# Kernel optimization log

Hardware: AMD Instinct MI355X
Metric: run time of the kernel (lower is better)

Reference implementation:

```python
import jax, jax.numpy as jnp
import numpy as np

T, H, I, E, Z, TOPK = 1024, 1024, 512, 32, 8, 4
ROUTED_SCALING = 1.0


def setup_inputs() -> dict:
    key = jax.random.key(0)
    k1, k2, k3, k4 = jax.random.split(key, 4)
    return {
        "hidden_states": jax.random.normal(k1, (T, H), jnp.float32),
        "router_w": jax.random.normal(k2, (E + Z, H), jnp.float32) * 0.02,
        "correction_bias": jnp.zeros((E + Z,), jnp.float32),
        "w_gate_up": jax.random.normal(k3, (E, 2 * I, H), jnp.float32) * 0.02,
        "w_down": jax.random.normal(k4, (E, H, I), jnp.float32) * 0.02,
        "top_k": TOPK,
    }


def reference(hidden_states, router_w, correction_bias, w_gate_up, w_down, top_k):
    # hidden_states: [T, H]; router_w: [E+Z, H]; w_gate_up: [E, 2I, H]; w_down: [E, H, I]
    t, h = hidden_states.shape
    e = w_gate_up.shape[0]
    i = w_down.shape[2]
    # --- router (float32, no bias; correction bias only affects selection) ---
    logits = jnp.einsum("th,eh->te", hidden_states.astype(jnp.float32), router_w)
    scores = jax.nn.softmax(logits, axis=-1)                     # [T, E+Z]
    _, idx = jax.lax.top_k(scores + correction_bias[None, :], top_k)  # [T, k]
    w = jnp.take_along_axis(scores, idx, axis=1) * ROUTED_SCALING     # renormalize=False
    # combine matrix [T, E+Z] (sparse top-k scattered dense)
    comb = jnp.zeros((t, scores.shape[1]), jnp.float32)
    comb = comb.at[jnp.arange(t)[:, None], idx].add(w)
    comb_routed = comb[:, :e].astype(hidden_states.dtype)        # [T, E]
    zero_w = comb[:, e:].sum(-1).astype(hidden_states.dtype)     # [T] identity zero-experts
    # --- grouped SiLU-gated expert MLPs (dense all-experts reference) ---
    gu = jnp.einsum("th,eih->eti", hidden_states, w_gate_up)     # [E, T, 2I]
    hmid = jax.nn.silu(gu[..., :i]) * gu[..., i:]                # [E, T, I]
    ye = jnp.einsum("eti,ehi->eth", hmid, w_down)                # [E, T, H]
    out = jnp.einsum("te,eth->th", comb_routed, ye)
    out = out + zero_w[:, None] * hidden_states
    return out
```

## Files before the change

### kernel.cpp

```cpp
#include <hip/hip_runtime.h>
#include <hip/hip_bf16.h>
#include <math.h>

#define TT   1024
#define HH   1024
#define II   512
#define EE   32
#define NE   40
#define TOPK 4
#define CAP  1024

#define GM  128
#define GNP 16
#define GK  32
#define KP  40
#define DN  32

typedef __attribute__((ext_vector_type(4))) short short4v;
typedef __attribute__((ext_vector_type(8))) short short8v;
typedef __attribute__((ext_vector_type(4))) float floatx4;

static __device__ __forceinline__ short f2bf(float f) {
    unsigned u = __float_as_uint(f);
    unsigned r = (u + 0x7fffu + ((u >> 16) & 1u)) >> 16;
    return (short)(r & 0xffffu);
}
static __device__ __forceinline__ float bf2f(short s) {
    return __uint_as_float(((unsigned)(unsigned short)s) << 16);
}
#if defined(__has_builtin)
#if __has_builtin(__builtin_amdgcn_cvt_pk_bf16_f32)
#define HAVE_PK_BF16 1
#endif
#endif
static __device__ __forceinline__ unsigned pk2(float a, float b) {
#ifdef HAVE_PK_BF16
    typedef __attribute__((ext_vector_type(2))) __bf16 bf2t;
    union { bf2t v; unsigned u; } cv;
    cv.v = __builtin_amdgcn_cvt_pk_bf16_f32(a, b);
    return cv.u;
#else
    return (unsigned)(unsigned short)f2bf(a) | ((unsigned)(unsigned short)f2bf(b) << 16);
#endif
}
static __device__ __forceinline__ short4v cvt4(float4 v) {
    union { unsigned u[2]; short4v s; } cv;
    cv.u[0] = pk2(v.x, v.y); cv.u[1] = pk2(v.z, v.w);
    return cv.s;
}

struct SMem {
    short As[GM * KP];
    short Bs[2 * GNP * KP];
    int   sl[GM];
    float wvs[GM];
};


__global__ __launch_bounds__(256, 4) void kA(
    const float* __restrict__ x, const float* __restrict__ rw,
    const float* __restrict__ bias, float* __restrict__ topk_w,
    float* __restrict__ zero_w, int* __restrict__ kexp,
    int* __restrict__ counts, int* __restrict__ slots, short* __restrict__ xb)
{
    const int bx = blockIdx.x, tid = threadIdx.x;
    const int lane = tid & 63;
    const int w    = tid >> 6;

    if (w < 2) {
        const int t = bx * 2 + w;
        float xv[16];
        #pragma unroll
        for (int i = 0; i < 16; ++i) xv[i] = x[(size_t)t * HH + 64 * i + lane];

        float mylogit = -INFINITY;
        for (int e0 = 0; e0 < NE; e0 += 4) {
            const float* r0 = rw + (size_t)e0 * HH;
            float p[4] = { 0.f, 0.f, 0.f, 0.f };
            #pragma unroll
            for (int i = 0; i < 16; ++i) {
                int h = 64 * i + lane;
                #pragma unroll
                for (int j = 0; j < 4; ++j) p[j] += xv[i] * r0[(size_t)j * HH + h];
            }
            #pragma unroll
            for (int j = 0; j < 4; ++j) {
                #pragma unroll
                for (int off = 32; off > 0; off >>= 1) p[j] += __shfl_xor(p[j], off);
                if (lane == e0 + j) mylogit = p[j];
            }
        }

        float m = mylogit;
        #pragma unroll
        for (int off = 32; off > 0; off >>= 1) m = fmaxf(m, __shfl_xor(m, off));
        float pexp = (lane < NE) ? expf(mylogit - m) : 0.f;
        float s = pexp;
        #pragma unroll
        for (int off = 32; off > 0; off >>= 1) s += __shfl_xor(s, off);
        const float score = pexp / s;

        float val = (lane < NE) ? score + bias[lane] : -INFINITY;
        int   kidx[TOPK];
        float kw[TOPK];
        #pragma unroll
        for (int k = 0; k < TOPK; ++k) {
            float v = val; int idx = lane;
            #pragma unroll
            for (int off = 32; off > 0; off >>= 1) {
                float ov = __shfl_xor(v, off);
                int   oi = __shfl_xor(idx, off);
                if (ov > v || (ov == v && oi < idx)) { v = ov; idx = oi; }
            }
            kidx[k] = idx;
            kw[k]   = __shfl(score, idx);
            if (lane == idx) val = -INFINITY;
        }

        if (lane == 0) {
            float zw = 0.f;
            #pragma unroll
            for (int k = 0; k < TOPK; ++k) {
                int slot = t * TOPK + k;
                topk_w[slot] = kw[k];
                kexp[slot]   = kidx[k];
                if (kidx[k] < EE) {
                    int pos = atomicAdd(&counts[kidx[k]], 1);
                    slots[kidx[k] * CAP + pos] = slot;
                } else {
                    zw += kw[k];
                }
            }
            zero_w[t] = zw;
        }
    } else {
        const int t = bx * 2 + (w - 2);
        const float4* xr = (const float4*)(x + (size_t)t * HH);
        short4v* xbr = (short4v*)(xb + (size_t)t * HH);
        #pragma unroll
        for (int i = 0; i < 4; ++i) xbr[lane + 64 * i] = cvt4(xr[lane + 64 * i]);
    }
}

__global__ __launch_bounds__(256, 4) void kB(
    const short* __restrict__ xb, const float* __restrict__ wgu,
    const int* __restrict__ counts, const int* __restrict__ slots,
    const float* __restrict__ topk_w, short* __restrict__ hmid)
{
    __shared__ SMem sm;
    const int bx = blockIdx.x, tid = threadIdx.x;
    const int e      = bx >> 5;
    const int c_base = (bx & 31) * GNP;
    const int cnt    = counts[e];
    const float* wb  = wgu + (size_t)e * (2 * II) * HH;

    const int lane = tid & 63;
    const int w    = tid >> 6;
    const int quad = lane >> 4;
    const int mcol = lane & 15;

    for (int m_base = 0; m_base < cnt; m_base += GM) {
        if (tid < GM) {
            int m = m_base + tid;
            int s = (m < cnt) ? slots[e * CAP + m] : -1;
            sm.sl[tid]  = s;
            sm.wvs[tid] = (s >= 0) ? topk_w[s] : 0.f;
        }
        __syncthreads();

        const int kcA = tid & 3;
        int rowA[2]; int slA[2]; const short* pA[2];
        #pragma unroll
        for (int it = 0; it < 2; ++it) {
            rowA[it] = (tid >> 2) + 64 * it;
            int s = sm.sl[rowA[it]];
            slA[it] = s;
            pA[it] = xb + (size_t)((s >= 0 ? s : 0) >> 2) * HH + kcA * 8;
        }
        const int kq   = tid & 7;
        const int rowB = tid >> 3;
        const int grow = (rowB < GNP) ? (c_base + rowB)
                                      : (II + c_base + (rowB - GNP));
        const float* pB = wb + (size_t)grow * HH + kq * 4;

        floatx4 accg[2] = {};
        floatx4 accu[2] = {};
        short8v pa[2]; float4 pb;
        const short8v szv = { 0,0,0,0,0,0,0,0 };

        #pragma unroll
        for (int it = 0; it < 2; ++it) pa[it] = (slA[it] >= 0) ? *(const short8v*)(pA[it]) : szv;
        pb = *(const float4*)(pB);

        for (int k0 = 0; k0 < HH; k0 += GK) {
            #pragma unroll
            for (int it = 0; it < 2; ++it) *(short8v*)&sm.As[rowA[it] * KP + kcA * 8] = pa[it];
            *(short4v*)&sm.Bs[rowB * KP + kq * 4] = cvt4(pb);
            __syncthreads();

            const int kn = k0 + GK;
            if (kn < HH) {
                #pragma unroll
                for (int it = 0; it < 2; ++it) pa[it] = (slA[it] >= 0) ? *(const short8v*)(pA[it] + kn) : szv;
                pb = *(const float4*)(pB + kn);
            }

            short8v a[2], bg, bu;
            #pragma unroll
            for (int i = 0; i < 2; ++i)
                a[i] = *(const short8v*)&sm.As[(w * 32 + i * 16 + mcol) * KP + quad * 8];
            bg = *(const short8v*)&sm.Bs[(mcol) * KP + quad * 8];
            bu = *(const short8v*)&sm.Bs[(GNP + mcol) * KP + quad * 8];
            #pragma unroll
            for (int i = 0; i < 2; ++i) {
                accg[i] = __builtin_amdgcn_mfma_f32_16x16x32_bf16(a[i], bg, accg[i], 0, 0, 0);
                accu[i] = __builtin_amdgcn_mfma_f32_16x16x32_bf16(a[i], bu, accu[i], 0, 0, 0);
            }
            __syncthreads();
        }

        #pragma unroll
        for (int i = 0; i < 2; ++i) {
            #pragma unroll
            for (int r = 0; r < 4; ++r) {
                int m = w * 32 + i * 16 + quad * 4 + r;
                int s = sm.sl[m];
                if (s < 0) continue;
                float g = accg[i][r], u = accu[i][r];
                float valf = sm.wvs[m] * g * u / (1.f + __expf(-g));
                hmid[(size_t)s * II + c_base + mcol] = f2bf(valf);
            }
        }
        __syncthreads();
    }
}

__global__ __launch_bounds__(256, 4) void kC(
    const short* __restrict__ hmid, const float* __restrict__ wd,
    const int* __restrict__ counts, const int* __restrict__ slots,
    short* __restrict__ ydown)
{
    __shared__ SMem sm;
    const int bx = blockIdx.x, tid = threadIdx.x;
    const int e      = bx >> 5;
    const int n_base = (bx & 31) * DN;
    const int cnt    = counts[e];
    const float* wb  = wd + (size_t)e * HH * II;

    const int lane = tid & 63;
    const int w    = tid >> 6;
    const int quad = lane >> 4;
    const int mcol = lane & 15;

    for (int m_base = 0; m_base < cnt; m_base += GM) {
        if (tid < GM) {
            int m = m_base + tid;
            sm.sl[tid] = (m < cnt) ? slots[e * CAP + m] : -1;
        }
        __syncthreads();

        const int kcA = tid & 3;
        int rowA[2]; int slA[2]; const short* pA[2];
        #pragma unroll
        for (int it = 0; it < 2; ++it) {
            rowA[it] = (tid >> 2) + 64 * it;
            int s = sm.sl[rowA[it]];
            slA[it] = s;
            pA[it] = hmid + (size_t)(s >= 0 ? s : 0) * II + kcA * 8;
        }
        const int kq   = tid & 7;
        const int rowB = tid >> 3;
        const float* pB = wb + (size_t)(n_base + rowB) * II + kq * 4;

        floatx4 acc[2][2] = {};
        short8v pa[2]; float4 pb;
        const short8v szv = { 0,0,0,0,0,0,0,0 };

        #pragma unroll
        for (int it = 0; it < 2; ++it) pa[it] = (slA[it] >= 0) ? *(const short8v*)(pA[it]) : szv;
        pb = *(const float4*)(pB);

        for (int k0 = 0; k0 < II; k0 += GK) {
            #pragma unroll
            for (int it = 0; it < 2; ++it) *(short8v*)&sm.As[rowA[it] * KP + kcA * 8] = pa[it];
            *(short4v*)&sm.Bs[rowB * KP + kq * 4] = cvt4(pb);
            __syncthreads();

            const int kn = k0 + GK;
            if (kn < II) {
                #pragma unroll
                for (int it = 0; it < 2; ++it) pa[it] = (slA[it] >= 0) ? *(const short8v*)(pA[it] + kn) : szv;
                pb = *(const float4*)(pB + kn);
            }

            short8v a[2], b[2];
            #pragma unroll
            for (int i = 0; i < 2; ++i)
                a[i] = *(const short8v*)&sm.As[(w * 32 + i * 16 + mcol) * KP + quad * 8];
            #pragma unroll
            for (int j = 0; j < 2; ++j)
                b[j] = *(const short8v*)&sm.Bs[(j * 16 + mcol) * KP + quad * 8];
            #pragma unroll
            for (int i = 0; i < 2; ++i)
                #pragma unroll
                for (int j = 0; j < 2; ++j)
                    acc[i][j] = __builtin_amdgcn_mfma_f32_16x16x32_bf16(a[i], b[j], acc[i][j], 0, 0, 0);
            __syncthreads();
        }

        #pragma unroll
        for (int i = 0; i < 2; ++i) {
            #pragma unroll
            for (int r = 0; r < 4; ++r) {
                int m = w * 32 + i * 16 + quad * 4 + r;
                int s = sm.sl[m];
                if (s < 0) continue;
                short* yrow = ydown + (size_t)s * HH + n_base;
                #pragma unroll
                for (int j = 0; j < 2; ++j)
                    yrow[j * 16 + mcol] = f2bf(acc[i][j][r]);
            }
        }
        __syncthreads();
    }
}

__global__ __launch_bounds__(256, 4) void kD(
    const float* __restrict__ x, const short* __restrict__ ydown,
    const int* __restrict__ kexp, const float* __restrict__ zero_w,
    float* __restrict__ out)
{
    const int bx = blockIdx.x, tid = threadIdx.x;
    const int t = bx;
    const float4 xvv = ((const float4*)(x + (size_t)t * HH))[tid];
    const float zw = zero_w[t];
    float4 o;
    o.x = zw * xvv.x; o.y = zw * xvv.y; o.z = zw * xvv.z; o.w = zw * xvv.w;
    #pragma unroll
    for (int k = 0; k < TOPK; ++k) {
        int slot = t * TOPK + k;
        if (kexp[slot] < EE) {
            short4v y = *(const short4v*)&ydown[(size_t)slot * HH + tid * 4];
            o.x += bf2f(y[0]); o.y += bf2f(y[1]);
            o.z += bf2f(y[2]); o.w += bf2f(y[3]);
        }
    }
    ((float4*)(out + (size_t)t * HH))[tid] = o;
}

extern "C" void kernel_launch(void* const* d_in, const int* in_sizes, int n_in,
                              void* d_out, int out_size, void* d_ws, size_t ws_size,
                              hipStream_t stream) {
    const float* x    = (const float*)d_in[0];
    const float* rw   = (const float*)d_in[1];
    const float* bias = (const float*)d_in[2];
    const float* wgu  = (const float*)d_in[3];
    const float* wd   = (const float*)d_in[4];
    float* out = (float*)d_out;

    char* ws = (char*)d_ws;
    int*   counts = (int*)ws;
    float* topk_w = (float*)(ws + 1024);
    float* zero_w = (float*)(ws + 17408);
    int*   kexp   = (int*)(ws + 21504);
    int*   slots  = (int*)(ws + 40960);
    short* xb     = (short*)(ws + 262144);
    short* hmid   = (short*)(ws + 2359296);
    short* ydown  = (short*)(ws + 6553600);

    hipMemsetAsync(counts, 0, EE * sizeof(int), stream);

    kA<<<dim3(512),  dim3(256), 0, stream>>>(x, rw, bias, topk_w, zero_w, kexp, counts, slots, xb);
    kB<<<dim3(1024), dim3(256), 0, stream>>>(xb, wgu, counts, slots, topk_w, hmid);
    kC<<<dim3(1024), dim3(256), 0, stream>>>(hmid, wd, counts, slots, ydown);
    kD<<<dim3(1024), dim3(256), 0, stream>>>(x, ydown, kexp, zero_w, out);
}
```

Measured before the change: 319.6 us.

## Double-buffer LDS tiles in expert GEMM kernels with one barrier per k-step

```diff
diff --git a/kernel.cpp b/kernel.cpp
--- a/kernel.cpp
+++ b/kernel.cpp
@@ -49,9 +49,9 @@
     return cv.s;
 }
 
-struct SMem {
-    short As[GM * KP];
-    short Bs[2 * GNP * KP];
+struct SMemB {
+    short As[2][GM * KP];
+    short Bs[2][2 * GNP * KP];
     int   sl[GM];
     float wvs[GM];
 };
@@ -147,7 +147,7 @@
     const int* __restrict__ counts, const int* __restrict__ slots,
     const float* __restrict__ topk_w, short* __restrict__ hmid)
 {
-    __shared__ SMem sm;
+    __shared__ SMemB sm;
     const int bx = blockIdx.x, tid = threadIdx.x;
     const int e      = bx >> 5;
     const int c_base = (bx & 31) * GNP;
@@ -158,6 +158,7 @@
     const int w    = tid >> 6;
     const int quad = lane >> 4;
     const int mcol = lane & 15;
+    constexpr int NT = HH / GK;
 
     for (int m_base = 0; m_base < cnt; m_base += GM) {
         if (tid < GM) {
@@ -169,13 +170,12 @@
         __syncthreads();
 
         const int kcA = tid & 3;
-        int rowA[2]; int slA[2]; const short* pA[2];
+        int rowA[2]; const short* pA[2];
         #pragma unroll
         for (int it = 0; it < 2; ++it) {
             rowA[it] = (tid >> 2) + 64 * it;
             int s = sm.sl[rowA[it]];
-            slA[it] = s;
-            pA[it] = xb + (size_t)((s >= 0 ? s : 0) >> 2) * HH + kcA * 8;
+            pA[it] = xb + (size_t)(((s >= 0 ? s : 0)) >> 2) * HH + kcA * 8;
         }
         const int kq   = tid & 7;
         const int rowB = tid >> 3;
@@ -185,38 +185,70 @@
 
         floatx4 accg[2] = {};
         floatx4 accu[2] = {};
-        short8v pa[2]; float4 pb;
-        const short8v szv = { 0,0,0,0,0,0,0,0 };
-
-        #pragma unroll
-        for (int it = 0; it < 2; ++it) pa[it] = (slA[it] >= 0) ? *(const short8v*)(pA[it]) : szv;
-        pb = *(const float4*)(pB);
-
-        for (int k0 = 0; k0 < HH; k0 += GK) {
-            #pragma unroll
-            for (int it = 0; it < 2; ++it) *(short8v*)&sm.As[rowA[it] * KP + kcA * 8] = pa[it];
-            *(short4v*)&sm.Bs[rowB * KP + kq * 4] = cvt4(pb);
-            __syncthreads();
-
-            const int kn = k0 + GK;
-            if (kn < HH) {
-                #pragma unroll
-                for (int it = 0; it < 2; ++it) pa[it] = (slA[it] >= 0) ? *(const short8v*)(pA[it] + kn) : szv;
-                pb = *(const float4*)(pB + kn);
-            }
-
-            short8v a[2], bg, bu;
-            #pragma unroll
-            for (int i = 0; i < 2; ++i)
-                a[i] = *(const short8v*)&sm.As[(w * 32 + i * 16 + mcol) * KP + quad * 8];
-            bg = *(const short8v*)&sm.Bs[(mcol) * KP + quad * 8];
-            bu = *(const short8v*)&sm.Bs[(GNP + mcol) * KP + quad * 8];
-            #pragma unroll
-            for (int i = 0; i < 2; ++i) {
-                accg[i] = __builtin_amdgcn_mfma_f32_16x16x32_bf16(a[i], bg, accg[i], 0, 0, 0);
-                accu[i] = __builtin_amdgcn_mfma_f32_16x16x32_bf16(a[i], bu, accu[i], 0, 0, 0);
-            }
-            __syncthreads();
+        short8v paA0, paA1, paB0, paB1; float4 pbA, pbB;
+
+        paA0 = *(const short8v*)(pA[0]);
+        paA1 = *(const short8v*)(pA[1]);
+        pbA  = *(const float4*)(pB);
+        paB0 = *(const short8v*)(pA[0] + GK);
+        paB1 = *(const short8v*)(pA[1] + GK);
+        pbB  = *(const float4*)(pB + GK);
+
+        *(short8v*)&sm.As[0][rowA[0] * KP + kcA * 8] = paA0;
+        *(short8v*)&sm.As[0][rowA[1] * KP + kcA * 8] = paA1;
+        *(short4v*)&sm.Bs[0][rowB * KP + kq * 4]     = cvt4(pbA);
+        asm volatile("s_waitcnt lgkmcnt(0)" ::: "memory");
+        __builtin_amdgcn_s_barrier();
+
+        for (int t0 = 0; t0 < NT; t0 += 2) {
+            {
+                const int ki = (t0 + 2) * GK;
+                if (ki < HH) {
+                    paA0 = *(const short8v*)(pA[0] + ki);
+                    paA1 = *(const short8v*)(pA[1] + ki);
+                    pbA  = *(const float4*)(pB + ki);
+                }
+                short8v a0 = *(const short8v*)&sm.As[0][(w * 32 + mcol) * KP + quad * 8];
+                short8v a1 = *(const short8v*)&sm.As[0][(w * 32 + 16 + mcol) * KP + quad * 8];
+                short8v bg = *(const short8v*)&sm.Bs[0][mcol * KP + quad * 8];
+                short8v bu = *(const short8v*)&sm.Bs[0][(GNP + mcol) * KP + quad * 8];
+                __builtin_amdgcn_s_setprio(1);
+                accg[0] = __builtin_amdgcn_mfma_f32_16x16x32_bf16(a0, bg, accg[0], 0, 0, 0);
+                accu[0] = __builtin_amdgcn_mfma_f32_16x16x32_bf16(a0, bu, accu[0], 0, 0, 0);
+                accg[1] = __builtin_amdgcn_mfma_f32_16x16x32_bf16(a1, bg, accg[1], 0, 0, 0);
+                accu[1] = __builtin_amdgcn_mfma_f32_16x16x32_bf16(a1, bu, accu[1], 0, 0, 0);
+                __builtin_amdgcn_s_setprio(0);
+                *(short8v*)&sm.As[1][rowA[0] * KP + kcA * 8] = paB0;
+                *(short8v*)&sm.As[1][rowA[1] * KP + kcA * 8] = paB1;
+                *(short4v*)&sm.Bs[1][rowB * KP + kq * 4]     = cvt4(pbB);
+                asm volatile("s_waitcnt lgkmcnt(0)" ::: "memory");
+                __builtin_amdgcn_s_barrier();
+            }
+            {
+                const int ki = (t0 + 3) * GK;
+                if (ki < HH) {
+                    paB0 = *(const short8v*)(pA[0] + ki);
+                    paB1 = *(const short8v*)(pA[1] + ki);
+                    pbB  = *(const float4*)(pB + ki);
+                }
+                short8v a0 = *(const short8v*)&sm.As[1][(w * 32 + mcol) * KP + quad * 8];
+                short8v a1 = *(const short8v*)&sm.As[1][(w * 32 + 16 + mcol) * KP + quad * 8];
+                short8v bg = *(const short8v*)&sm.Bs[1][mcol * KP + quad * 8];
+                short8v bu = *(const short8v*)&sm.Bs[1][(GNP + mcol) * KP + quad * 8];
+                __builtin_amdgcn_s_setprio(1);
+                accg[0] = __builtin_amdgcn_mfma_f32_16x16x32_bf16(a0, bg, accg[0], 0, 0, 0);
+                accu[0] = __builtin_amdgcn_mfma_f32_16x16x32_bf16(a0, bu, accu[0], 0, 0, 0);
+                accg[1] = __builtin_amdgcn_mfma_f32_16x16x32_bf16(a1, bg, accg[1], 0, 0, 0);
+                accu[1] = __builtin_amdgcn_mfma_f32_16x16x32_bf16(a1, bu, accu[1], 0, 0, 0);
+                __builtin_amdgcn_s_setprio(0);
+                if (t0 + 2 < NT) {
+                    *(short8v*)&sm.As[0][rowA[0] * KP + kcA * 8] = paA0;
+                    *(short8v*)&sm.As[0][rowA[1] * KP + kcA * 8] = paA1;
+                    *(short4v*)&sm.Bs[0][rowB * KP + kq * 4]     = cvt4(pbA);
+                    asm volatile("s_waitcnt lgkmcnt(0)" ::: "memory");
+                    __builtin_amdgcn_s_barrier();
+                }
+            }
         }
 
         #pragma unroll
@@ -226,7 +258,8 @@
                 int m = w * 32 + i * 16 + quad * 4 + r;
                 int s = sm.sl[m];
                 if (s < 0) continue;
-                float g = accg[i][r], u = accu[i][r];
+                float g = (i == 0) ? accg[0][r] : accg[1][r];
+                float u = (i == 0) ? accu[0][r] : accu[1][r];
                 float valf = sm.wvs[m] * g * u / (1.f + __expf(-g));
                 hmid[(size_t)s * II + c_base + mcol] = f2bf(valf);
             }
@@ -240,7 +273,7 @@
     const int* __restrict__ counts, const int* __restrict__ slots,
     short* __restrict__ ydown)
 {
-    __shared__ SMem sm;
+    __shared__ SMemB sm;
     const int bx = blockIdx.x, tid = threadIdx.x;
     const int e      = bx >> 5;
     const int n_base = (bx & 31) * DN;
@@ -251,6 +284,7 @@
     const int w    = tid >> 6;
     const int quad = lane >> 4;
     const int mcol = lane & 15;
+    constexpr int NT = II / GK;
 
     for (int m_base = 0; m_base < cnt; m_base += GM) {
         if (tid < GM) {
@@ -260,52 +294,82 @@
         __syncthreads();
 
         const int kcA = tid & 3;
-        int rowA[2]; int slA[2]; const short* pA[2];
+        int rowA[2]; const short* pA[2];
         #pragma unroll
         for (int it = 0; it < 2; ++it) {
             rowA[it] = (tid >> 2) + 64 * it;
             int s = sm.sl[rowA[it]];
-            slA[it] = s;
             pA[it] = hmid + (size_t)(s >= 0 ? s : 0) * II + kcA * 8;
         }
         const int kq   = tid & 7;
         const int rowB = tid >> 3;
         const float* pB = wb + (size_t)(n_base + rowB) * II + kq * 4;
 
-        floatx4 acc[2][2] = {};
-        short8v pa[2]; float4 pb;
-        const short8v szv = { 0,0,0,0,0,0,0,0 };
-
-        #pragma unroll
-        for (int it = 0; it < 2; ++it) pa[it] = (slA[it] >= 0) ? *(const short8v*)(pA[it]) : szv;
-        pb = *(const float4*)(pB);
-
-        for (int k0 = 0; k0 < II; k0 += GK) {
-            #pragma unroll
-            for (int it = 0; it < 2; ++it) *(short8v*)&sm.As[rowA[it] * KP + kcA * 8] = pa[it];
-            *(short4v*)&sm.Bs[rowB * KP + kq * 4] = cvt4(pb);
-            __syncthreads();
-
-            const int kn = k0 + GK;
-            if (kn < II) {
-                #pragma unroll
-                for (int it = 0; it < 2; ++it) pa[it] = (slA[it] >= 0) ? *(const short8v*)(pA[it] + kn) : szv;
-                pb = *(const float4*)(pB + kn);
-            }
-
-            short8v a[2], b[2];
-            #pragma unroll
-            for (int i = 0; i < 2; ++i)
-                a[i] = *(const short8v*)&sm.As[(w * 32 + i * 16 + mcol) * KP + quad * 8];
-            #pragma unroll
-            for (int j = 0; j < 2; ++j)
-                b[j] = *(const short8v*)&sm.Bs[(j * 16 + mcol) * KP + quad * 8];
-            #pragma unroll
-            for (int i = 0; i < 2; ++i)
-                #pragma unroll
-                for (int j = 0; j < 2; ++j)
-                    acc[i][j] = __builtin_amdgcn_mfma_f32_16x16x32_bf16(a[i], b[j], acc[i][j], 0, 0, 0);
-            __syncthreads();
+        floatx4 acc00 = {}, acc01 = {}, acc10 = {}, acc11 = {};
+        short8v paA0, paA1, paB0, paB1; float4 pbA, pbB;
+
+        paA0 = *(const short8v*)(pA[0]);
+        paA1 = *(const short8v*)(pA[1]);
+        pbA  = *(const float4*)(pB);
+        paB0 = *(const short8v*)(pA[0] + GK);
+        paB1 = *(const short8v*)(pA[1] + GK);
+        pbB  = *(const float4*)(pB + GK);
+
+        *(short8v*)&sm.As[0][rowA[0] * KP + kcA * 8] = paA0;
+        *(short8v*)&sm.As[0][rowA[1] * KP + kcA * 8] = paA1;
+        *(short4v*)&sm.Bs[0][rowB * KP + kq * 4]     = cvt4(pbA);
+        asm volatile("s_waitcnt lgkmcnt(0)" ::: "memory");
+        __builtin_amdgcn_s_barrier();
+
+        for (int t0 = 0; t0 < NT; t0 += 2) {
+            {
+                const int ki = (t0 + 2) * GK;
+                if (ki < II) {
+                    paA0 = *(const short8v*)(pA[0] + ki);
+                    paA1 = *(const short8v*)(pA[1] + ki);
+                    pbA  = *(const float4*)(pB + ki);
+                }
+                short8v a0 = *(const short8v*)&sm.As[0][(w * 32 + mcol) * KP + quad * 8];
+                short8v a1 = *(const short8v*)&sm.As[0][(w * 32 + 16 + mcol) * KP + quad * 8];
+                short8v b0 = *(const short8v*)&sm.Bs[0][mcol * KP + quad * 8];
+                short8v b1 = *(const short8v*)&sm.Bs[0][(16 + mcol) * KP + quad * 8];
+                __builtin_amdgcn_s_setprio(1);
+                acc00 = __builtin_amdgcn_mfma_f32_16x16x32_bf16(a0, b0, acc00, 0, 0, 0);
+                acc01 = __builtin_amdgcn_mfma_f32_16x16x32_bf16(a0, b1, acc01, 0, 0, 0);
+                acc10 = __builtin_amdgcn_mfma_f32_16x16x32_bf16(a1, b0, acc10, 0, 0, 0);
+                acc11 = __builtin_amdgcn_mfma_f32_16x16x32_bf16(a1, b1, acc11, 0, 0, 0);
+                __builtin_amdgcn_s_setprio(0);
+                *(short8v*)&sm.As[1][rowA[0] * KP + kcA * 8] = paB0;
+                *(short8v*)&sm.As[1][rowA[1] * KP + kcA * 8] = paB1;
+                *(short4v*)&sm.Bs[1][rowB * KP + kq * 4]     = cvt4(pbB);
+                asm volatile("s_waitcnt lgkmcnt(0)" ::: "memory");
+                __builtin_amdgcn_s_barrier();
+            }
+            {
+                const int ki = (t0 + 3) * GK;
+                if (ki < II) {
+                    paB0 = *(const short8v*)(pA[0] + ki);
+                    paB1 = *(const short8v*)(pA[1] + ki);
+                    pbB  = *(const float4*)(pB + ki);
+                }
+                short8v a0 = *(const short8v*)&sm.As[1][(w * 32 + mcol) * KP + quad * 8];
+                short8v a1 = *(const short8v*)&sm.As[1][(w * 32 + 16 + mcol) * KP + quad * 8];
+                short8v b0 = *(const short8v*)&sm.Bs[1][mcol * KP + quad * 8];
+                short8v b1 = *(const short8v*)&sm.Bs[1][(16 + mcol) * KP + quad * 8];
+                __builtin_amdgcn_s_setprio(1);
+                acc00 = __builtin_amdgcn_mfma_f32_16x16x32_bf16(a0, b0, acc00, 0, 0, 0);
+                acc01 = __builtin_amdgcn_mfma_f32_16x16x32_bf16(a0, b1, acc01, 0, 0, 0);
+                acc10 = __builtin_amdgcn_mfma_f32_16x16x32_bf16(a1, b0, acc10, 0, 0, 0);
+                acc11 = __builtin_amdgcn_mfma_f32_16x16x32_bf16(a1, b1, acc11, 0, 0, 0);
+                __builtin_amdgcn_s_setprio(0);
+                if (t0 + 2 < NT) {
+                    *(short8v*)&sm.As[0][rowA[0] * KP + kcA * 8] = paA0;
+                    *(short8v*)&sm.As[0][rowA[1] * KP + kcA * 8] = paA1;
+                    *(short4v*)&sm.Bs[0][rowB * KP + kq * 4]     = cvt4(pbA);
+                    asm volatile("s_waitcnt lgkmcnt(0)" ::: "memory");
+                    __builtin_amdgcn_s_barrier();
+                }
+            }
         }
 
         #pragma unroll
@@ -316,9 +380,10 @@
                 int s = sm.sl[m];
                 if (s < 0) continue;
                 short* yrow = ydown + (size_t)s * HH + n_base;
-                #pragma unroll
-                for (int j = 0; j < 2; ++j)
-                    yrow[j * 16 + mcol] = f2bf(acc[i][j][r]);
+                float v0 = (i == 0) ? acc00[r] : acc10[r];
+                float v1 = (i == 0) ? acc01[r] : acc11[r];
+                yrow[mcol]      = f2bf(v0);
+                yrow[16 + mcol] = f2bf(v1);
             }
         }
         __syncthreads();
```

Result: no change. 322.5 us (+0.9%).

## Drop LDS staging in expert GEMMs, load MFMA fragments directly from global

Applied to the files above, without the earlier changes.

```diff
diff --git a/kernel.cpp b/kernel.cpp
--- a/kernel.cpp
+++ b/kernel.cpp
@@ -11,10 +11,7 @@
 #define CAP  1024
 
 #define GM  128
-#define GNP 16
 #define GK  32
-#define KP  40
-#define DN  32
 
 typedef __attribute__((ext_vector_type(4))) short short4v;
 typedef __attribute__((ext_vector_type(8))) short short8v;
@@ -48,13 +45,11 @@
     cv.u[0] = pk2(v.x, v.y); cv.u[1] = pk2(v.z, v.w);
     return cv.s;
 }
-
-struct SMem {
-    short As[GM * KP];
-    short Bs[2 * GNP * KP];
-    int   sl[GM];
-    float wvs[GM];
-};
+static __device__ __forceinline__ short8v pack8(float4 f0, float4 f1) {
+    union { short4v h[2]; short8v v; } u;
+    u.h[0] = cvt4(f0); u.h[1] = cvt4(f1);
+    return u.v;
+}
 
 
 __global__ __launch_bounds__(256, 4) void kA(
@@ -142,186 +137,228 @@
     }
 }
 
-__global__ __launch_bounds__(256, 4) void kB(
+__global__ __launch_bounds__(256, 2) void kB(
     const short* __restrict__ xb, const float* __restrict__ wgu,
     const int* __restrict__ counts, const int* __restrict__ slots,
     const float* __restrict__ topk_w, short* __restrict__ hmid)
 {
-    __shared__ SMem sm;
+    __shared__ int   ssl[GM];
+    __shared__ float swv[GM];
     const int bx = blockIdx.x, tid = threadIdx.x;
-    const int e      = bx >> 5;
-    const int c_base = (bx & 31) * GNP;
+    const int e      = bx >> 4;
+    const int c_base = (bx & 15) * 32;
     const int cnt    = counts[e];
     const float* wb  = wgu + (size_t)e * (2 * II) * HH;
 
     const int lane = tid & 63;
     const int w    = tid >> 6;
+    const int wm   = w >> 1;
+    const int wn   = w & 1;
     const int quad = lane >> 4;
     const int mcol = lane & 15;
+    constexpr int NT = HH / GK;
+
+    const float* pG = wb + (size_t)(c_base + wn * 16 + mcol) * HH + quad * 8;
+    const float* pU = wb + (size_t)(II + c_base + wn * 16 + mcol) * HH + quad * 8;
 
     for (int m_base = 0; m_base < cnt; m_base += GM) {
+        __syncthreads();
         if (tid < GM) {
             int m = m_base + tid;
             int s = (m < cnt) ? slots[e * CAP + m] : -1;
-            sm.sl[tid]  = s;
-            sm.wvs[tid] = (s >= 0) ? topk_w[s] : 0.f;
+            ssl[tid] = s;
+            swv[tid] = (s >= 0) ? topk_w[s] : 0.f;
         }
         __syncthreads();
 
-        const int kcA = tid & 3;
-        int rowA[2]; int slA[2]; const short* pA[2];
-        #pragma unroll
-        for (int it = 0; it < 2; ++it) {
-            rowA[it] = (tid >> 2) + 64 * it;
-            int s = sm.sl[rowA[it]];
-            slA[it] = s;
-            pA[it] = xb + (size_t)((s >= 0 ? s : 0) >> 2) * HH + kcA * 8;
-        }
-        const int kq   = tid & 7;
-        const int rowB = tid >> 3;
-        const int grow = (rowB < GNP) ? (c_base + rowB)
-                                      : (II + c_base + (rowB - GNP));
-        const float* pB = wb + (size_t)grow * HH + kq * 4;
-
-        floatx4 accg[2] = {};
-        floatx4 accu[2] = {};
-        short8v pa[2]; float4 pb;
-        const short8v szv = { 0,0,0,0,0,0,0,0 };
-
-        #pragma unroll
-        for (int it = 0; it < 2; ++it) pa[it] = (slA[it] >= 0) ? *(const short8v*)(pA[it]) : szv;
-        pb = *(const float4*)(pB);
-
-        for (int k0 = 0; k0 < HH; k0 += GK) {
-            #pragma unroll
-            for (int it = 0; it < 2; ++it) *(short8v*)&sm.As[rowA[it] * KP + kcA * 8] = pa[it];
-            *(short4v*)&sm.Bs[rowB * KP + kq * 4] = cvt4(pb);
-            __syncthreads();
-
-            const int kn = k0 + GK;
-            if (kn < HH) {
-                #pragma unroll
-                for (int it = 0; it < 2; ++it) pa[it] = (slA[it] >= 0) ? *(const short8v*)(pA[it] + kn) : szv;
-                pb = *(const float4*)(pB + kn);
-            }
-
-            short8v a[2], bg, bu;
-            #pragma unroll
-            for (int i = 0; i < 2; ++i)
-                a[i] = *(const short8v*)&sm.As[(w * 32 + i * 16 + mcol) * KP + quad * 8];
-            bg = *(const short8v*)&sm.Bs[(mcol) * KP + quad * 8];
-            bu = *(const short8v*)&sm.Bs[(GNP + mcol) * KP + quad * 8];
-            #pragma unroll
-            for (int i = 0; i < 2; ++i) {
-                accg[i] = __builtin_amdgcn_mfma_f32_16x16x32_bf16(a[i], bg, accg[i], 0, 0, 0);
-                accu[i] = __builtin_amdgcn_mfma_f32_16x16x32_bf16(a[i], bu, accu[i], 0, 0, 0);
-            }
-            __syncthreads();
-        }
-
-        #pragma unroll
-        for (int i = 0; i < 2; ++i) {
+        const short* pA0, *pA1, *pA2, *pA3;
+        {
+            int s0 = ssl[wm * 64 +  0 + mcol];
+            int s1 = ssl[wm * 64 + 16 + mcol];
+            int s2 = ssl[wm * 64 + 32 + mcol];
+            int s3 = ssl[wm * 64 + 48 + mcol];
+            pA0 = xb + (size_t)(((s0 >= 0 ? s0 : 0)) >> 2) * HH + quad * 8;
+            pA1 = xb + (size_t)(((s1 >= 0 ? s1 : 0)) >> 2) * HH + quad * 8;
+            pA2 = xb + (size_t)(((s2 >= 0 ? s2 : 0)) >> 2) * HH + quad * 8;
+            pA3 = xb + (size_t)(((s3 >= 0 ? s3 : 0)) >> 2) * HH + quad * 8;
+        }
+
+        floatx4 accg[4] = {};
+        floatx4 accu[4] = {};
+        short8v aA0, aA1, aA2, aA3, aB0, aB1, aB2, aB3;
+        float4  gA0, gA1, uA0, uA1, gB0, gB1, uB0, uB1;
+
+        aA0 = *(const short8v*)(pA0);
+        aA1 = *(const short8v*)(pA1);
+        aA2 = *(const short8v*)(pA2);
+        aA3 = *(const short8v*)(pA3);
+        gA0 = *(const float4*)(pG);     gA1 = *(const float4*)(pG + 4);
+        uA0 = *(const float4*)(pU);     uA1 = *(const float4*)(pU + 4);
+
+        for (int t = 0; t < NT; t += 2) {
+            const int k1 = (t + 1) * GK;
+            aB0 = *(const short8v*)(pA0 + k1);
+            aB1 = *(const short8v*)(pA1 + k1);
+            aB2 = *(const short8v*)(pA2 + k1);
+            aB3 = *(const short8v*)(pA3 + k1);
+            gB0 = *(const float4*)(pG + k1); gB1 = *(const float4*)(pG + k1 + 4);
+            uB0 = *(const float4*)(pU + k1); uB1 = *(const float4*)(pU + k1 + 4);
+            {
+                short8v bg = pack8(gA0, gA1), bu = pack8(uA0, uA1);
+                accg[0] = __builtin_amdgcn_mfma_f32_16x16x32_bf16(aA0, bg, accg[0], 0, 0, 0);
+                accu[0] = __builtin_amdgcn_mfma_f32_16x16x32_bf16(aA0, bu, accu[0], 0, 0, 0);
+                accg[1] = __builtin_amdgcn_mfma_f32_16x16x32_bf16(aA1, bg, accg[1], 0, 0, 0);
+                accu[1] = __builtin_amdgcn_mfma_f32_16x16x32_bf16(aA1, bu, accu[1], 0, 0, 0);
+                accg[2] = __builtin_amdgcn_mfma_f32_16x16x32_bf16(aA2, bg, accg[2], 0, 0, 0);
+                accu[2] = __builtin_amdgcn_mfma_f32_16x16x32_bf16(aA2, bu, accu[2], 0, 0, 0);
+                accg[3] = __builtin_amdgcn_mfma_f32_16x16x32_bf16(aA3, bg, accg[3], 0, 0, 0);
+                accu[3] = __builtin_amdgcn_mfma_f32_16x16x32_bf16(aA3, bu, accu[3], 0, 0, 0);
+            }
+            const int k2 = (t + 2) * GK;
+            if (k2 < HH) {
+                aA0 = *(const short8v*)(pA0 + k2);
+                aA1 = *(const short8v*)(pA1 + k2);
+                aA2 = *(const short8v*)(pA2 + k2);
+                aA3 = *(const short8v*)(pA3 + k2);
+                gA0 = *(const float4*)(pG + k2); gA1 = *(const float4*)(pG + k2 + 4);
+                uA0 = *(const float4*)(pU + k2); uA1 = *(const float4*)(pU + k2 + 4);
+            }
+            {
+                short8v bg = pack8(gB0, gB1), bu = pack8(uB0, uB1);
+                accg[0] = __builtin_amdgcn_mfma_f32_16x16x32_bf16(aB0, bg, accg[0], 0, 0, 0);
+                accu[0] = __builtin_amdgcn_mfma_f32_16x16x32_bf16(aB0, bu, accu[0], 0, 0, 0);
+                accg[1] = __builtin_amdgcn_mfma_f32_16x16x32_bf16(aB1, bg, accg[1], 0, 0, 0);
+                accu[1] = __builtin_amdgcn_mfma_f32_16x16x32_bf16(aB1, bu, accu[1], 0, 0, 0);
+                accg[2] = __builtin_amdgcn_mfma_f32_16x16x32_bf16(aB2, bg, accg[2], 0, 0, 0);
+                accu[2] = __builtin_amdgcn_mfma_f32_16x16x32_bf16(aB2, bu, accu[2], 0, 0, 0);
+                accg[3] = __builtin_amdgcn_mfma_f32_16x16x32_bf16(aB3, bg, accg[3], 0, 0, 0);
+                accu[3] = __builtin_amdgcn_mfma_f32_16x16x32_bf16(aB3, bu, accu[3], 0, 0, 0);
+            }
+        }
+
+        #pragma unroll
+        for (int i = 0; i < 4; ++i) {
             #pragma unroll
             for (int r = 0; r < 4; ++r) {
-                int m = w * 32 + i * 16 + quad * 4 + r;
-                int s = sm.sl[m];
+                int m = wm * 64 + i * 16 + quad * 4 + r;
+                int s = ssl[m];
                 if (s < 0) continue;
                 float g = accg[i][r], u = accu[i][r];
-                float valf = sm.wvs[m] * g * u / (1.f + __expf(-g));
-                hmid[(size_t)s * II + c_base + mcol] = f2bf(valf);
-            }
-        }
-        __syncthreads();
+                float valf = swv[m] * g * u / (1.f + __expf(-g));
+                hmid[(size_t)s * II + c_base + wn * 16 + mcol] = f2bf(valf);
+            }
+        }
     }
 }
 
-__global__ __launch_bounds__(256, 4) void kC(
+__global__ __launch_bounds__(256, 2) void kC(
     const short* __restrict__ hmid, const float* __restrict__ wd,
     const int* __restrict__ counts, const int* __restrict__ slots,
     short* __restrict__ ydown)
 {
-    __shared__ SMem sm;
+    __shared__ int ssl[GM];
     const int bx = blockIdx.x, tid = threadIdx.x;
-    const int e      = bx >> 5;
-    const int n_base = (bx & 31) * DN;
+    const int e      = bx >> 4;
+    const int n_base = (bx & 15) * 64;
     const int cnt    = counts[e];
     const float* wb  = wd + (size_t)e * HH * II;
 
     const int lane = tid & 63;
     const int w    = tid >> 6;
+    const int wm   = w >> 1;
+    const int wn   = w & 1;
     const int quad = lane >> 4;
     const int mcol = lane & 15;
+    constexpr int NT = II / GK;
+
+    const float* pW0 = wb + (size_t)(n_base + wn * 32 +      mcol) * II + quad * 8;
+    const float* pW1 = wb + (size_t)(n_base + wn * 32 + 16 + mcol) * II + quad * 8;
 
     for (int m_base = 0; m_base < cnt; m_base += GM) {
+        __syncthreads();
         if (tid < GM) {
             int m = m_base + tid;
-            sm.sl[tid] = (m < cnt) ? slots[e * CAP + m] : -1;
+            ssl[tid] = (m < cnt) ? slots[e * CAP + m] : -1;
         }
         __syncthreads();
 
-        const int kcA = tid & 3;
-        int rowA[2]; int slA[2]; const short* pA[2];
-        #pragma unroll
-        for (int it = 0; it < 2; ++it) {
-            rowA[it] = (tid >> 2) + 64 * it;
-            int s = sm.sl[rowA[it]];
-            slA[it] = s;
-            pA[it] = hmid + (size_t)(s >= 0 ? s : 0) * II + kcA * 8;
-        }
-        const int kq   = tid & 7;
-        const int rowB = tid >> 3;
-        const float* pB = wb + (size_t)(n_base + rowB) * II + kq * 4;
-
-        floatx4 acc[2][2] = {};
-        short8v pa[2]; float4 pb;
-        const short8v szv = { 0,0,0,0,0,0,0,0 };
-
-        #pragma unroll
-        for (int it = 0; it < 2; ++it) pa[it] = (slA[it] >= 0) ? *(const short8v*)(pA[it]) : szv;
-        pb = *(const float4*)(pB);
-
-        for (int k0 = 0; k0 < II; k0 += GK) {
-            #pragma unroll
-            for (int it = 0; it < 2; ++it) *(short8v*)&sm.As[rowA[it] * KP + kcA * 8] = pa[it];
-            *(short4v*)&sm.Bs[rowB * KP + kq * 4] = cvt4(pb);
-            __syncthreads();
-
-            const int kn = k0 + GK;
-            if (kn < II) {
-                #pragma unroll
-                for (int it = 0; it < 2; ++it) pa[it] = (slA[it] >= 0) ? *(const short8v*)(pA[it] + kn) : szv;
-                pb = *(const float4*)(pB + kn);
-            }
-
-            short8v a[2], b[2];
-            #pragma unroll
-            for (int i = 0; i < 2; ++i)
-                a[i] = *(const short8v*)&sm.As[(w * 32 + i * 16 + mcol) * KP + quad * 8];
-            #pragma unroll
-            for (int j = 0; j < 2; ++j)
-                b[j] = *(const short8v*)&sm.Bs[(j * 16 + mcol) * KP + quad * 8];
-            #pragma unroll
-            for (int i = 0; i < 2; ++i)
-                #pragma unroll
-                for (int j = 0; j < 2; ++j)
-                    acc[i][j] = __builtin_amdgcn_mfma_f32_16x16x32_bf16(a[i], b[j], acc[i][j], 0, 0, 0);
-            __syncthreads();
-        }
-
-        #pragma unroll
-        for (int i = 0; i < 2; ++i) {
+        const short* pA0, *pA1, *pA2, *pA3;
+        {
+            int s0 = ssl[wm * 64 +  0 + mcol];
+            int s1 = ssl[wm * 64 + 16 + mcol];
+            int s2 = ssl[wm * 64 + 32 + mcol];
+            int s3 = ssl[wm * 64 + 48 + mcol];
+            pA0 = hmid + (size_t)(s0 >= 0 ? s0 : 0) * II + quad * 8;
+            pA1 = hmid + (size_t)(s1 >= 0 ? s1 : 0) * II + quad * 8;
+            pA2 = hmid + (size_t)(s2 >= 0 ? s2 : 0) * II + quad * 8;
+            pA3 = hmid + (size_t)(s3 >= 0 ? s3 : 0) * II + quad * 8;
+        }
+
+        floatx4 acc0[4] = {};
+        floatx4 acc1[4] = {};
+        short8v aA0, aA1, aA2, aA3, aB0, aB1, aB2, aB3;
+        float4  w0A0, w0A1, w1A0, w1A1, w0B0, w0B1, w1B0, w1B1;
+
+        aA0 = *(const short8v*)(pA0);
+        aA1 = *(const short8v*)(pA1);
+        aA2 = *(const short8v*)(pA2);
+        aA3 = *(const short8v*)(pA3);
+        w0A0 = *(const float4*)(pW0);     w0A1 = *(const float4*)(pW0 + 4);
+        w1A0 = *(const float4*)(pW1);     w1A1 = *(const float4*)(pW1 + 4);
+
+        for (int t = 0; t < NT; t += 2) {
+            const int k1 = (t + 1) * GK;
+            aB0 = *(const short8v*)(pA0 + k1);
+            aB1 = *(const short8v*)(pA1 + k1);
+            aB2 = *(const short8v*)(pA2 + k1);
+            aB3 = *(const short8v*)(pA3 + k1);
+            w0B0 = *(const float4*)(pW0 + k1); w0B1 = *(const float4*)(pW0 + k1 + 4);
+            w1B0 = *(const float4*)(pW1 + k1); w1B1 = *(const float4*)(pW1 + k1 + 4);
+            {
+                short8v b0 = pack8(w0A0, w0A1), b1 = pack8(w1A0, w1A1);
+                acc0[0] = __builtin_amdgcn_mfma_f32_16x16x32_bf16(aA0, b0, acc0[0], 0, 0, 0);
+                acc1[0] = __builtin_amdgcn_mfma_f32_16x16x32_bf16(aA0, b1, acc1[0], 0, 0, 0);
+                acc0[1] = __builtin_amdgcn_mfma_f32_16x16x32_bf16(aA1, b0, acc0[1], 0, 0, 0);
+                acc1[1] = __builtin_amdgcn_mfma_f32_16x16x32_bf16(aA1, b1, acc1[1], 0, 0, 0);
+                acc0[2] = __builtin_amdgcn_mfma_f32_16x16x32_bf16(aA2, b0, acc0[2], 0, 0, 0);
+                acc1[2] = __builtin_amdgcn_mfma_f32_16x16x32_bf16(aA2, b1, acc1[2], 0, 0, 0);
+                acc0[3] = __builtin_amdgcn_mfma_f32_16x16x32_bf16(aA3, b0, acc0[3], 0, 0, 0);
+                acc1[3] = __builtin_amdgcn_mfma_f32_16x16x32_bf16(aA3, b1, acc1[3], 0, 0, 0);
+            }
+            const int k2 = (t + 2) * GK;
+            if (k2 < II) {
+                aA0 = *(const short8v*)(pA0 + k2);
+                aA1 = *(const short8v*)(pA1 + k2);
+                aA2 = *(const short8v*)(pA2 + k2);
+                aA3 = *(const short8v*)(pA3 + k2);
+                w0A0 = *(const float4*)(pW0 + k2); w0A1 = *(const float4*)(pW0 + k2 + 4);
+                w1A0 = *(const float4*)(pW1 + k2); w1A1 = *(const float4*)(pW1 + k2 + 4);
+            }
+            {
+                short8v b0 = pack8(w0B0, w0B1), b1 = pack8(w1B0, w1B1);
+                acc0[0] = __builtin_amdgcn_mfma_f32_16x16x32_bf16(aB0, b0, acc0[0], 0, 0, 0);
+                acc1[0] = __builtin_amdgcn_mfma_f32_16x16x32_bf16(aB0, b1, acc1[0], 0, 0, 0);
+                acc0[1] = __builtin_amdgcn_mfma_f32_16x16x32_bf16(aB1, b0, acc0[1], 0, 0, 0);
+                acc1[1] = __builtin_amdgcn_mfma_f32_16x16x32_bf16(aB1, b1, acc1[1], 0, 0, 0);
+                acc0[2] = __builtin_amdgcn_mfma_f32_16x16x32_bf16(aB2, b0, acc0[2], 0, 0, 0);
+                acc1[2] = __builtin_amdgcn_mfma_f32_16x16x32_bf16(aB2, b1, acc1[2], 0, 0, 0);
+                acc0[3] = __builtin_amdgcn_mfma_f32_16x16x32_bf16(aB3, b0, acc0[3], 0, 0, 0);
+                acc1[3] = __builtin_amdgcn_mfma_f32_16x16x32_bf16(aB3, b1, acc1[3], 0, 0, 0);
+            }
+        }
+
+        #pragma unroll
+        for (int i = 0; i < 4; ++i) {
             #pragma unroll
             for (int r = 0; r < 4; ++r) {
-                int m = w * 32 + i * 16 + quad * 4 + r;
-                int s = sm.sl[m];
+                int m = wm * 64 + i * 16 + quad * 4 + r;
+                int s = ssl[m];
                 if (s < 0) continue;
-                short* yrow = ydown + (size_t)s * HH + n_base;
-                #pragma unroll
-                for (int j = 0; j < 2; ++j)
-                    yrow[j * 16 + mcol] = f2bf(acc[i][j][r]);
-            }
-        }
-        __syncthreads();
+                short* yrow = ydown + (size_t)s * HH + n_base + wn * 32;
+                yrow[mcol]      = f2bf(acc0[i][r]);
+                yrow[16 + mcol] = f2bf(acc1[i][r]);
+            }
+        }
     }
 }
 
@@ -370,8 +407,8 @@
 
     hipMemsetAsync(counts, 0, EE * sizeof(int), stream);
 
-    kA<<<dim3(512),  dim3(256), 0, stream>>>(x, rw, bias, topk_w, zero_w, kexp, counts, slots, xb);
-    kB<<<dim3(1024), dim3(256), 0, stream>>>(xb, wgu, counts, slots, topk_w, hmid);
-    kC<<<dim3(1024), dim3(256), 0, stream>>>(hmid, wd, counts, slots, ydown);
+    kA<<<dim3(512), dim3(256), 0, stream>>>(x, rw, bias, topk_w, zero_w, kexp, counts, slots, xb);
+    kB<<<dim3(512), dim3(256), 0, stream>>>(xb, wgu, counts, slots, topk_w, hmid);
+    kC<<<dim3(512), dim3(256), 0, stream>>>(hmid, wd, counts, slots, ydown);
     kD<<<dim3(1024), dim3(256), 0, stream>>>(x, ydown, kexp, zero_w, out);
 }
```

Measured after the change: 338.3 us. 1.06x slower.
